# Performance work log

Measured on AMD Instinct MI355X. Metric: run time of the kernel, lower is better.

## Reference

```python
import jax, jax.numpy as jnp
from jax import lax
import numpy as np

B, NR, NC, FEAT = 8, 1024, 1024, 768
N = NR + NC
HID, GATD, GRUD = 256, 128, 64
NEG = -9e15  # matches -9000000000000000.0 in torch source


def setup_inputs() -> dict:
    key = jax.random.key(0)
    ks = jax.random.split(key, 24)
    s = 0.02
    nrm = lambda k, shp: jax.random.normal(k, shp, jnp.float32) * s
    z = lambda shp: jnp.zeros(shp, jnp.float32)
    inp = {}
    inp['req_nodes'] = jax.random.normal(ks[0], (B, NR, FEAT), jnp.float32)
    inp['code_nodes'] = jax.random.normal(ks[1], (B, NC, FEAT), jnp.float32)
    inp['alignment_matrix'] = jax.random.bernoulli(ks[2], 0.05, (B, N, N)).astype(jnp.float32)
    inp['total_nodes'] = jax.random.randint(ks[3], (B,), N // 2, N + 1).astype(jnp.int32)
    # feature_projection
    inp['W_proj'] = nrm(ks[4], (HID, FEAT)); inp['b_proj'] = z((HID,))
    # GAT layer 1 (HID->HID), attention weight a is Linear(2*HID, 1, bias=False)
    inp['W_g1'] = nrm(ks[5], (HID, HID)); inp['b_g1'] = z((HID,)); inp['a_g1'] = nrm(ks[6], (2 * HID,))
    # GAT layer 2 (HID->GATD)
    inp['W_g2'] = nrm(ks[7], (GATD, HID)); inp['b_g2'] = z((GATD,)); inp['a_g2'] = nrm(ks[8], (2 * GATD,))
    # bidirectional GRU (torch layout: [3H, in], gates r|z|n)
    inp['Wih_f'] = nrm(ks[9], (3 * GRUD, GATD)); inp['Whh_f'] = nrm(ks[10], (3 * GRUD, GRUD))
    inp['bih_f'] = z((3 * GRUD,)); inp['bhh_f'] = z((3 * GRUD,))
    inp['Wih_b'] = nrm(ks[11], (3 * GRUD, GATD)); inp['Whh_b'] = nrm(ks[12], (3 * GRUD, GRUD))
    inp['bih_b'] = z((3 * GRUD,)); inp['bhh_b'] = z((3 * GRUD,))
    inp['W_fus'] = nrm(ks[13], (GRUD, 2 * GRUD)); inp['b_fus'] = z((GRUD,))
    inp['W_c1'] = nrm(ks[14], (HID // 2, GRUD)); inp['b_c1'] = z((HID // 2,))
    inp['W_c2'] = nrm(ks[15], (1, HID // 2)); inp['b_c2'] = z((1,))
    return inp


def _gat_layer(x, adj, mask, W, b, a):
    # h: [B, N, D]
    h = x @ W.T + b
    D = h.shape[-1]
    # attention(concat(h_i, h_j)) == a[:D]@h_i + a[D:]@h_j -> never materialize [B,N,N,2D]
    s_src = h @ a[:D]   # [B, N]
    s_dst = h @ a[D:]   # [B, N]
    e = jax.nn.leaky_relu(s_src[:, :, None] + s_dst[:, None, :], 0.01)  # [B,N,N]
    att = jax.nn.softmax(jnp.where(adj > 0, e, NEG), axis=-1)
    out = jnp.einsum('bij,bjd->bid', att, h)
    return out * mask[..., None]


def _gru_dir(xproj, Whh, bhh, reverse):
    # xproj: [B, T, 3H] = x @ Wih.T + bih (precomputed)
    Bv, H = xproj.shape[0], Whh.shape[1]
    def step(h, xt):
        gh = h @ Whh.T + bhh
        ir, iz, inn = jnp.split(xt, 3, axis=-1)
        hr, hz, hn = jnp.split(gh, 3, axis=-1)
        r = jax.nn.sigmoid(ir + hr)
        zt = jax.nn.sigmoid(iz + hz)
        n = jnp.tanh(inn + r * hn)
        hnew = (1.0 - zt) * n + zt * h
        return hnew, hnew
    h0 = jnp.zeros((Bv, H), xproj.dtype)
    _, ys = lax.scan(step, h0, jnp.swapaxes(xproj, 0, 1), reverse=reverse)
    return jnp.swapaxes(ys, 0, 1)  # [B, T, H]


def _forward(req_nodes, code_nodes, alignment_matrix, total_nodes,
             W_proj, b_proj, W_g1, b_g1, a_g1, W_g2, b_g2, a_g2,
             Wih_f, Whh_f, bih_f, bhh_f, Wih_b, Whh_b, bih_b, bhh_b,
             W_fus, b_fus, W_c1, b_c1, W_c2, b_c2):
    x = jnp.concatenate([req_nodes, code_nodes], axis=1)        # [B, N, FEAT]
    proj = jax.nn.relu(x @ W_proj.T + b_proj)                   # dropout is eval-mode identity
    Nt = proj.shape[1]
    mask = (jnp.arange(Nt)[None, :] < total_nodes[:, None]).astype(proj.dtype)  # [B, N]
    g1 = _gat_layer(proj, alignment_matrix, mask, W_g1, b_g1, a_g1)
    g1 = jax.nn.relu(g1) * mask[..., None]
    gat_out = _gat_layer(g1, alignment_matrix, mask, W_g2, b_g2, a_g2)
    gat_out = gat_out * mask[..., None]  # extra masking as in torch source (idempotent)
    gf = _gru_dir(gat_out @ Wih_f.T + bih_f, Whh_f, bhh_f, reverse=False)
    gb = _gru_dir(gat_out @ Wih_b.T + bih_b, Whh_b, bhh_b, reverse=True)
    gru_out = jnp.concatenate([gf, gb], axis=-1) * mask[..., None]  # [B, N, 2*GRUD]
    fused = gru_out @ W_fus.T + b_fus                               # [B, N, GRUD]
    pooled = jnp.mean(fused, axis=1)  # AdaptiveAvgPool1d(1) over seq dim
    h1 = jax.nn.relu(pooled @ W_c1.T + b_c1)
    out = jax.nn.sigmoid(h1 @ W_c2.T + b_c2)  # [B, 1]
    return out


def reference(req_nodes, code_nodes, alignment_matrix, total_nodes,
              W_proj, b_proj, W_g1, b_g1, a_g1, W_g2, b_g2, a_g2,
              Wih_f, Whh_f, bih_f, bhh_f, Wih_b, Whh_b, bih_b, bhh_b,
              W_fus, b_fus, W_c1, b_c1, W_c2, b_c2):
    return _forward(req_nodes, code_nodes, alignment_matrix, total_nodes,
                    W_proj, b_proj, W_g1, b_g1, a_g1, W_g2, b_g2, a_g2,
                    Wih_f, Whh_f, bih_f, bhh_f, Wih_b, Whh_b, bih_b, bhh_b,
                    W_fus, b_fus, W_c1, b_c1, W_c2, b_c2)
```

## Files before the change

### kernel.cpp

```cpp
#include <hip/hip_runtime.h>
#include <stdint.h>

#define EMAX 256

typedef short bf16x8 __attribute__((ext_vector_type(8)));
typedef float f32x4 __attribute__((ext_vector_type(4)));
typedef _Float16 h2_t __attribute__((ext_vector_type(2)));

__device__ __forceinline__ uint16_t f2bf(float f) {
    union { float f; uint32_t u; } v; v.f = f;
    uint32_t u = v.u;
    uint32_t r = (u + 0x7FFFu + ((u >> 16) & 1u)) >> 16;
    return (uint16_t)r;
}
__device__ __forceinline__ float bf2f(uint16_t h) {
    union { uint32_t u; float f; } v; v.u = ((uint32_t)h) << 16;
    return v.f;
}
__device__ __forceinline__ h2_t u2h2(uint32_t u) {
    union { uint32_t u; h2_t h; } v; v.u = u;
    return v.h;
}

__global__ __launch_bounds__(256) void k_prep(const float* __restrict__ req, const float* __restrict__ code,
                                              uint16_t* __restrict__ X,
                                              const float* wp, const float* wg1, const float* wg2,
                                              const float* wif, const float* wib,
                                              const float* whf, const float* whb,
                                              const float* bihf, const float* bihb,
                                              uint16_t* op, uint16_t* og1, uint16_t* og2,
                                              uint16_t* oifb, _Float16* ohf, _Float16* ohb, float* bihfb,
                                              float* __restrict__ Sz,
                                              const float* __restrict__ adj,
                                              uint16_t* __restrict__ eidx, int* __restrict__ ecnt) {
    int blk = blockIdx.x;
    int tid = threadIdx.x;
    if (blk < 16384) {
        int b = blk >> 11, n = blk & 2047;
        if (tid < 192) {
            const float4* src4 = (const float4*)((n < 1024) ? (req  + ((size_t)(b*1024 + n)) * 768)
                                                            : (code + ((size_t)(b*1024 + (n-1024))) * 768));
            ushort4* dst4 = (ushort4*)(X + (size_t)blk * 768);
            float4 v = src4[tid];
            ushort4 p;
            p.x = f2bf(v.x); p.y = f2bf(v.y); p.z = f2bf(v.z); p.w = f2bf(v.w);
            dst4[tid] = p;
        }
    } else if (blk < 16384 + 768) {
        int i = (blk - 16384) * 256 + tid;
        if (i < 196608) op[i]  = f2bf(wp[i]);
        if (i < 65536)  og1[i] = f2bf(wg1[i]);
        if (i < 32768)  og2[i] = f2bf(wg2[i]);
        if (i < 24576)  { oifb[i] = f2bf(wif[i]); oifb[24576 + i] = f2bf(wib[i]); }
        if (i < 12288)  { ohf[i] = (_Float16)whf[i]; ohb[i] = (_Float16)whb[i]; }
        if (i < 192)    { bihfb[i] = bihf[i]; bihfb[192 + i] = bihb[i]; }
        if (i < 1024)   Sz[i] = 0.f;
    } else {
        int row  = (blk - 17152) * 4 + (tid >> 6);
        int lane = tid & 63;
        const float* arow = adj + (size_t)row * 2048;
        uint16_t* out = eidx + (size_t)row * EMAX;
        int base = 0;
        for (int c = 0; c < 32; ++c) {
            int j = c * 64 + lane;
            float v = arow[j];
            unsigned long long m = __ballot(v > 0.0f);
            if (v > 0.0f) {
                int pos = base + __popcll(m & ((1ull << lane) - 1ull));
                if (pos < EMAX) out[pos] = (uint16_t)j;
            }
            base += __popcll(m);
        }
        if (lane == 0) ecnt[row] = (base < EMAX) ? base : EMAX;
    }
}

template<int ACT, int MODE>
__global__ __launch_bounds__(256) void k_gemm(const uint16_t* __restrict__ A,
                                              const uint16_t* __restrict__ Bw,
                                              const float* __restrict__ bias,
                                              void* __restrict__ Cv, void* __restrict__ Cv2,
                                              int M, int N, int K) {
    __shared__ __align__(16) uint16_t As[64 * 64];
    __shared__ __align__(16) uint16_t Bs[64 * 64];
    int tid = threadIdx.x;
    int n0 = blockIdx.x * 64, m0 = blockIdx.y * 64;
    int wave = tid >> 6, lane = tid & 63;
    int quad = lane >> 4, l16 = lane & 15;
    f32x4 acc[4] = {};
    int ar = tid >> 3;
    int ac = (tid & 7) * 8;
    for (int kb = 0; kb < K; kb += 64) {
        *(uint4*)&As[ar * 64 + ac]        = *(const uint4*)(A  + (size_t)(m0 + ar)      * K + kb + ac);
        *(uint4*)&As[(ar + 32) * 64 + ac] = *(const uint4*)(A  + (size_t)(m0 + ar + 32) * K + kb + ac);
        *(uint4*)&Bs[ar * 64 + ac]        = *(const uint4*)(Bw + (size_t)(n0 + ar)      * K + kb + ac);
        *(uint4*)&Bs[(ar + 32) * 64 + ac] = *(const uint4*)(Bw + (size_t)(n0 + ar + 32) * K + kb + ac);
        __syncthreads();
#pragma unroll
        for (int kk = 0; kk < 64; kk += 32) {
            bf16x8 af = *(bf16x8*)&As[(wave * 16 + l16) * 64 + kk + quad * 8];
#pragma unroll
            for (int c = 0; c < 4; ++c) {
                bf16x8 bfr = *(bf16x8*)&Bs[(c * 16 + l16) * 64 + kk + quad * 8];
                acc[c] = __builtin_amdgcn_mfma_f32_16x16x32_bf16(af, bfr, acc[c], 0, 0, 0);
            }
        }
        __syncthreads();
    }
#pragma unroll
    for (int c = 0; c < 4; ++c) {
        int col = n0 + c * 16 + l16;
        float bv = bias ? bias[col] : 0.f;
#pragma unroll
        for (int rg = 0; rg < 4; ++rg) {
            int row = m0 + wave * 16 + quad * 4 + rg;
            float v = acc[c][rg] + bv;
            if (ACT == 1) v = fmaxf(v, 0.f);
            if (MODE == 1)      ((uint16_t*)Cv)[(size_t)row * N + col] = f2bf(v);
            else if (MODE == 0) ((float*)Cv)[(size_t)row * N + col] = v;
            else {
                int tc = (col < 192) ? col : col - 192;
                int dc = (tc & 63) * 4 + (tc >> 6);
                float* dst = (col < 192) ? (float*)Cv : (float*)Cv2;
                dst[(size_t)row * 256 + dc] = v;
            }
        }
    }
}

template<int D>
__global__ __launch_bounds__(256) void k_attvec(const uint16_t* __restrict__ H,
                                                const float* __restrict__ a,
                                                float* __restrict__ ssrc,
                                                float* __restrict__ sdst) {
    int row  = blockIdx.x * 4 + (threadIdx.x >> 6);
    int lane = threadIdx.x & 63;
    constexpr int PER = D >> 6;
    const uint32_t* hr = (const uint32_t*)(H + (size_t)row * D + lane * PER);
    float s0 = 0.f, s1 = 0.f;
#pragma unroll
    for (int q = 0; q < PER / 2; ++q) {
        uint32_t hv = hr[q];
        int d = lane * PER + q * 2;
        float h0 = bf2f((uint16_t)hv), h1 = bf2f((uint16_t)(hv >> 16));
        s0 += h0 * a[d] + h1 * a[d + 1];
        s1 += h0 * a[D + d] + h1 * a[D + d + 1];
    }
    for (int off = 32; off; off >>= 1) { s0 += __shfl_down(s0, off); s1 += __shfl_down(s1, off); }
    if (lane == 0) { ssrc[row] = s0; sdst[row] = s1; }
}

#define ACC4(hv, wv) { \
    a0 = fmaf(wv, bf2f((uint16_t)(hv).x), a0); \
    a1 = fmaf(wv, bf2f((uint16_t)((hv).x >> 16)), a1); \
    a2 = fmaf(wv, bf2f((uint16_t)(hv).y), a2); \
    a3 = fmaf(wv, bf2f((uint16_t)((hv).y >> 16)), a3); }

template<int D, int LAYER1>
__global__ __launch_bounds__(256) void k_agg(const uint16_t* __restrict__ H,
                                             const float* __restrict__ ssrc,
                                             const float* __restrict__ sdst,
                                             const uint16_t* __restrict__ eidx,
                                             const int* __restrict__ ecnt,
                                             const int* __restrict__ total,
                                             uint16_t* __restrict__ out) {
    constexpr int LPG = (D == 256) ? 64 : 32;
    constexpr int G   = 64 / LPG;
    constexpr int RS  = D / 4;
    __shared__ __align__(16) uint2 ew[4][EMAX];
    int tid  = threadIdx.x;
    int wid  = tid >> 6, lane = tid & 63;
    int grp  = lane / LPG;
    int c    = lane % LPG;
    int b    = blockIdx.x & 7;
    int i    = ((blockIdx.x >> 3) << 2) + wid;
    int row  = (b << 11) + i;
    uint2* orow = (uint2*)(out + (size_t)row * D);
    if (i >= total[b]) {
        if (grp == 0) { uint2 z; z.x = 0u; z.y = 0u; orow[c] = z; }
        return;
    }
    int cnt = ecnt[row];
    const uint2* H2 = (const uint2*)(H + (size_t)b * 2048 * D);
    float a0 = 0.f, a1 = 0.f, a2 = 0.f, a3 = 0.f;
    if (cnt > 0) {
        float sv = ssrc[row];
        const uint16_t* er = eidx + (size_t)row * EMAX;
        int   jj[4]; float ee[4];
#pragma unroll
        for (int k = 0; k < 4; ++k) {
            int t = lane + 64 * k;
            int j = (t < cnt) ? (int)er[t] : 0;
            float x = sv + sdst[b * 2048 + j];
            float e = (x > 0.f) ? x : 0.01f * x;
            if (t >= cnt) e = -1e30f;
            jj[k] = j; ee[k] = e;
        }
        float m = fmaxf(fmaxf(ee[0], ee[1]), fmaxf(ee[2], ee[3]));
#pragma unroll
        for (int off = 32; off; off >>= 1) m = fmaxf(m, __shfl_xor(m, off));
        float w[4]; float s = 0.f;
#pragma unroll
        for (int k = 0; k < 4; ++k) { w[k] = __expf(ee[k] - m); s += w[k]; }
#pragma unroll
        for (int off = 32; off; off >>= 1) s += __shfl_xor(s, off);
        float inv = 1.f / s;
#pragma unroll
        for (int k = 0; k < 4; ++k) {
            uint2 p; p.x = (uint32_t)jj[k]; p.y = __float_as_uint(w[k] * inv);
            ew[wid][lane + 64 * k] = p;
        }
        asm volatile("s_waitcnt lgkmcnt(0)" ::: "memory");
        constexpr int EPB = 4 * G;
        int cntP = (cnt + EPB - 1) & ~(EPB - 1);
        if constexpr (G == 1) {
            for (int t = 0; t < cntP; t += 4) {
                uint2 e0 = ew[wid][t + 0], e1 = ew[wid][t + 1];
                uint2 e2 = ew[wid][t + 2], e3 = ew[wid][t + 3];
                uint2 h0 = H2[(size_t)e0.x * RS + c];
                uint2 h1 = H2[(size_t)e1.x * RS + c];
                uint2 h2 = H2[(size_t)e2.x * RS + c];
                uint2 h3 = H2[(size_t)e3.x * RS + c];
                ACC4(h0, __uint_as_float(e0.y));
                ACC4(h1, __uint_as_float(e1.y));
                ACC4(h2, __uint_as_float(e2.y));
                ACC4(h3, __uint_as_float(e3.y));
            }
        } else {
            for (int t = 0; t < cntP; t += 8) {
                uint2 e0 = ew[wid][t + 0 + grp], e1 = ew[wid][t + 2 + grp];
                uint2 e2 = ew[wid][t + 4 + grp], e3 = ew[wid][t + 6 + grp];
                uint2 h0 = H2[(size_t)e0.x * RS + c];
                uint2 h1 = H2[(size_t)e1.x * RS + c];
                uint2 h2 = H2[(size_t)e2.x * RS + c];
                uint2 h3 = H2[(size_t)e3.x * RS + c];
                ACC4(h0, __uint_as_float(e0.y));
                ACC4(h1, __uint_as_float(e1.y));
                ACC4(h2, __uint_as_float(e2.y));
                ACC4(h3, __uint_as_float(e3.y));
            }
        }
    } else {
        for (int t = grp; t < 2048; t += G) {
            uint2 hv = H2[(size_t)t * RS + c];
            ACC4(hv, 1.f);
        }
        a0 *= (1.f / 2048.f); a1 *= (1.f / 2048.f);
        a2 *= (1.f / 2048.f); a3 *= (1.f / 2048.f);
    }
    if constexpr (G == 2) {
        a0 += __shfl_xor(a0, 32); a1 += __shfl_xor(a1, 32);
        a2 += __shfl_xor(a2, 32); a3 += __shfl_xor(a3, 32);
    }
    if (LAYER1) {
        a0 = fmaxf(a0, 0.f); a1 = fmaxf(a1, 0.f);
        a2 = fmaxf(a2, 0.f); a3 = fmaxf(a3, 0.f);
    }
    if (grp == 0) {
        uint2 pk;
        pk.x = (uint32_t)f2bf(a0) | ((uint32_t)f2bf(a1) << 16);
        pk.y = (uint32_t)f2bf(a2) | ((uint32_t)f2bf(a3) << 16);
        orow[c] = pk;
    }
}

#define CHUNKS 16
#define CLEN   128
#define WARM   64
#define FDOT2(acc, p, wq) acc = __builtin_amdgcn_fdot2(p, u2h2(wq), acc, false)
#define DOTBLK(hq, q) { \
    h2_t p0 = u2h2(hq.x), p1 = u2h2(hq.y), p2 = u2h2(hq.z), p3 = u2h2(hq.w); \
    FDOT2(ar0, p0, wr[4*q+0]); FDOT2(ar1, p1, wr[4*q+1]); FDOT2(ar2, p2, wr[4*q+2]); FDOT2(ar3, p3, wr[4*q+3]); \
    FDOT2(az0, p0, wz[4*q+0]); FDOT2(az1, p1, wz[4*q+1]); FDOT2(az2, p2, wz[4*q+2]); FDOT2(az3, p3, wz[4*q+3]); \
    FDOT2(an0, p0, wn[4*q+0]); FDOT2(an1, p1, wn[4*q+1]); FDOT2(an2, p2, wn[4*q+2]); FDOT2(an3, p3, wn[4*q+3]); }
#define GRU_STEP(xq) { \
    uint4 h0 = hv4[0], h1 = hv4[1], h2v = hv4[2], h3 = hv4[3]; \
    uint4 h4 = hv4[4], h5 = hv4[5], h6 = hv4[6], h7 = hv4[7]; \
    float ar0 = br, ar1 = 0.f, ar2 = 0.f, ar3 = 0.f; \
    float az0 = bz, az1 = 0.f, az2 = 0.f, az3 = 0.f; \
    float an0 = bn, an1 = 0.f, an2 = 0.f, an3 = 0.f; \
    DOTBLK(h0, 0) DOTBLK(h1, 1) DOTBLK(h2v, 2) DOTBLK(h3, 3) \
    DOTBLK(h4, 4) DOTBLK(h5, 5) DOTBLK(h6, 6) DOTBLK(h7, 7) \
    float ghr = (ar0 + ar1) + (ar2 + ar3); \
    float ghz = (az0 + az1) + (az2 + az3); \
    float ghn = (an0 + an1) + (an2 + an3); \
    float er = __expf(-(xq.x + ghr)); \
    float r = __builtin_amdgcn_rcpf(1.f + er); \
    float ez = __expf(-(xq.y + ghz)); \
    float z = __builtin_amdgcn_rcpf(1.f + ez); \
    float nv = fmaf(r, ghn, xq.z); \
    float en = __expf(-2.f * nv); \
    float n = fmaf(-2.f, __builtin_amdgcn_rcpf(1.f + en), 1.f); \
    hj = fmaf(z, hj - n, n); \
    sj += (t < Tcur) ? hj : 0.f; \
    hb[j] = (_Float16)hj; \
    asm volatile("" ::: "memory"); \
    t += dt; }

__global__ __attribute__((amdgpu_flat_work_group_size(64, 64), amdgpu_waves_per_eu(1, 1)))
void k_gru(const float* __restrict__ XPf, const float* __restrict__ XPb,
           const _Float16* __restrict__ WhF, const _Float16* __restrict__ WhB,
           const float* __restrict__ bhh_f, const float* __restrict__ bhh_b,
           const int* __restrict__ total,
           float* __restrict__ S) {
    int blk   = blockIdx.x;
    int chunk = blk & (CHUNKS - 1);
    int sc    = blk >> 4;
    int dir   = sc >> 3;
    int b     = sc & 7;
    int j     = threadIdx.x;
    const float* XP  = dir ? XPb : XPf;
    const uint32_t* Wd = (const uint32_t*)(dir ? WhB : WhF);
    const float* bhh = dir ? bhh_b : bhh_f;
    uint32_t wr[32], wz[32], wn[32];
#pragma unroll
    for (int c = 0; c < 32; ++c) {
        wr[c] = Wd[(size_t)(      j) * 32 + c];
        wz[c] = Wd[(size_t)( 64 + j) * 32 + c];
        wn[c] = Wd[(size_t)(128 + j) * 32 + c];
    }
    float br = bhh[j], bz = bhh[64 + j], bn = bhh[128 + j];
    __shared__ __align__(16) _Float16 hbuf[64];
    _Float16* hb = hbuf;
    hb[j] = (_Float16)0.f;
    asm volatile("s_waitcnt lgkmcnt(0)" ::: "memory");
    float hj = 0.f, sj = 0.f;
    int Tb = total[b];
    int s0 = chunk * CLEN - WARM;
    int W0 = WARM;
    if (s0 < 0) { s0 = 0; W0 = 0; }
    const float4* xbase = (const float4*)(XP + (size_t)b * 2048 * 256) + j;
    int xstep = dir ? -64 : 64;
    const float4* xptr = xbase + (size_t)(dir ? (2047 - s0) : s0) * 64;
    float4 x0 = *xptr; xptr += xstep;
    float4 x1 = *xptr; xptr += xstep;
    float4 x2 = *xptr; xptr += xstep;
    float4 x3 = *xptr; xptr += xstep;
    int t = dir ? (2047 - s0) : s0, dt = dir ? -1 : 1;
    const uint4* hv4 = (const uint4*)hb;
    int Tcur = -1;
    for (int su = 0; su < W0; su += 4) {
        GRU_STEP(x0) x0 = *xptr; xptr += xstep;
        GRU_STEP(x1) x1 = *xptr; xptr += xstep;
        GRU_STEP(x2) x2 = *xptr; xptr += xstep;
        GRU_STEP(x3) x3 = *xptr; xptr += xstep;
    }
    Tcur = Tb;
    for (int su = 0; su < CLEN; su += 4) {
        GRU_STEP(x0) x0 = *xptr; xptr += xstep;
        GRU_STEP(x1) x1 = *xptr; xptr += xstep;
        GRU_STEP(x2) x2 = *xptr; xptr += xstep;
        GRU_STEP(x3) x3 = *xptr; xptr += xstep;
    }
    atomicAdd(&S[b * 128 + dir * 64 + j], sj);
}

__global__ __launch_bounds__(128) void k_final(const float* __restrict__ S,
                                               const float* __restrict__ Wfus, const float* __restrict__ bfus,
                                               const float* __restrict__ Wc1, const float* __restrict__ bc1,
                                               const float* __restrict__ Wc2, const float* __restrict__ bc2,
                                               float* __restrict__ out) {
    __shared__ float pool[64];
    __shared__ float red[128];
    int tid = threadIdx.x;
    for (int b = 0; b < 8; ++b) {
        if (tid < 64) {
            float a = 0.f;
            for (int jj = 0; jj < 128; ++jj) a += S[b * 128 + jj] * Wfus[tid * 128 + jj];
            pool[tid] = bfus[tid] + a * (1.f / 2048.f);
        }
        __syncthreads();
        float a1 = 0.f;
        for (int d = 0; d < 64; ++d) a1 += pool[d] * Wc1[tid * 64 + d];
        float h = fmaxf(a1 + bc1[tid], 0.f);
        red[tid] = h * Wc2[tid];
        __syncthreads();
        for (int s = 64; s; s >>= 1) { if (tid < s) red[tid] += red[tid + s]; __syncthreads(); }
        if (tid == 0) out[b] = 1.f / (1.f + __expf(-(red[0] + bc2[0])));
        __syncthreads();
    }
}

extern "C" void kernel_launch(void* const* d_in, const int* in_sizes, int n_in,
                              void* d_out, int out_size, void* d_ws, size_t ws_size,
                              hipStream_t stream) {
    (void)in_sizes; (void)n_in; (void)out_size; (void)ws_size;
    const float* req   = (const float*)d_in[0];
    const float* code  = (const float*)d_in[1];
    const float* adj   = (const float*)d_in[2];
    const int*   total = (const int*)  d_in[3];
    const float* W_proj = (const float*)d_in[4];
    const float* b_proj = (const float*)d_in[5];
    const float* W_g1   = (const float*)d_in[6];
    const float* b_g1   = (const float*)d_in[7];
    const float* a_g1   = (const float*)d_in[8];
    const float* W_g2   = (const float*)d_in[9];
    const float* b_g2   = (const float*)d_in[10];
    const float* a_g2   = (const float*)d_in[11];
    const float* Wih_f  = (const float*)d_in[12];
    const float* Whh_f  = (const float*)d_in[13];
    const float* bih_f  = (const float*)d_in[14];
    const float* bhh_f  = (const float*)d_in[15];
    const float* Wih_b  = (const float*)d_in[16];
    const float* Whh_b  = (const float*)d_in[17];
    const float* bih_b  = (const float*)d_in[18];
    const float* bhh_b  = (const float*)d_in[19];
    const float* W_fus  = (const float*)d_in[20];
    const float* b_fus  = (const float*)d_in[21];
    const float* W_c1   = (const float*)d_in[22];
    const float* b_c1   = (const float*)d_in[23];
    const float* W_c2   = (const float*)d_in[24];
    const float* b_c2   = (const float*)d_in[25];

    char* ws = (char*)d_ws;
    uint16_t* Xbf  = (uint16_t*)(ws + 0);
    float*    XPf  = (float*)(ws + 4096);
    float*    XPb  = (float*)(ws + 4096 + 16777216 + 4096);
    uint16_t* EIDX = (uint16_t*)(ws + 25169920);
    uint16_t* WPb  = (uint16_t*)(ws + 33570816);
    uint16_t* WG1b = (uint16_t*)(ws + 33964032);
    uint16_t* WG2b = (uint16_t*)(ws + 34095104);
    uint16_t* WIFB = (uint16_t*)(ws + 34160640);
    uint16_t* Pbf  = (uint16_t*)(ws + 34262016);
    uint16_t* H1bf = (uint16_t*)(ws + 42650624);
    uint16_t* H2bf = (uint16_t*)(ws + 42650624);
    uint16_t* G2bf = (uint16_t*)(ws + 46844928);
    uint16_t* G1bf = (uint16_t*)(ws + 51039232);
    int*      ECNT = (int*)     (ws + 59427840);
    float* s1src = (float*)(ws + 59493376);
    float* s1dst = (float*)(ws + 59558912);
    float* s2src = (float*)(ws + 59624448);
    float* s2dst = (float*)(ws + 59689984);
    float* Sbuf  = (float*)(ws + 59755520);
    _Float16* WhFh = (_Float16*)(ws + 59759616);
    _Float16* WhBh = (_Float16*)(ws + 59784192);
    float* BIHFB   = (float*)(ws + 59808768);

    k_prep<<<21248, 256, 0, stream>>>(req, code, Xbf,
                                      W_proj, W_g1, W_g2, Wih_f, Wih_b, Whh_f, Whh_b, bih_f, bih_b,
                                      WPb, WG1b, WG2b, WIFB, WhFh, WhBh, BIHFB, Sbuf,
                                      adj, EIDX, ECNT);

    k_gemm<1, 1><<<dim3(4, 256), 256, 0, stream>>>(Xbf, WPb, b_proj, Pbf, nullptr, 16384, 256, 768);

    k_gemm<0, 1><<<dim3(4, 256), 256, 0, stream>>>(Pbf, WG1b, b_g1, H1bf, nullptr, 16384, 256, 256);
    k_attvec<256><<<4096, 256, 0, stream>>>(H1bf, a_g1, s1src, s1dst);
    k_agg<256, 1><<<4096, 256, 0, stream>>>(H1bf, s1src, s1dst, EIDX, ECNT, total, G1bf);

    k_gemm<0, 1><<<dim3(2, 256), 256, 0, stream>>>(G1bf, WG2b, b_g2, H2bf, nullptr, 16384, 128, 256);
    k_attvec<128><<<4096, 256, 0, stream>>>(H2bf, a_g2, s2src, s2dst);
    k_agg<128, 0><<<4096, 256, 0, stream>>>(H2bf, s2src, s2dst, EIDX, ECNT, total, G2bf);

    k_gemm<0, 2><<<dim3(6, 256), 256, 0, stream>>>(G2bf, WIFB, BIHFB, XPf, XPb, 16384, 384, 128);

    k_gru<<<256, 64, 0, stream>>>(XPf, XPb, WhFh, WhBh, bhh_f, bhh_b, total, Sbuf);

    k_final<<<1, 128, 0, stream>>>(Sbuf, W_fus, b_fus, W_c1, b_c1, W_c2, b_c2, (float*)d_out);
}
```

Baseline: 557.4 us.

## Fuse fp32-to-bf16 input conversion into projection GEMM and co-schedule adjacency compaction

Removes the separate pass that converted req/code features to a bf16 staging buffer. The projection GEMM now loads fp32 rows directly and packs them to bf16 with v_cvt_pk_bf16_f32 while filling shared memory. Adjacency edge-list compaction moves into the same launch as extra blocks, and each lane loads all 32 adjacency values up front. This drops a write and re-read of the staging buffer, but the GEMM's global loads double in width and weight prep becomes its own small kernel.

```diff
diff --git a/kernel.cpp b/kernel.cpp
--- a/kernel.cpp
+++ b/kernel.cpp
@@ -21,57 +21,111 @@
     union { uint32_t u; h2_t h; } v; v.u = u;
     return v.h;
 }
-
-__global__ __launch_bounds__(256) void k_prep(const float* __restrict__ req, const float* __restrict__ code,
-                                              uint16_t* __restrict__ X,
-                                              const float* wp, const float* wg1, const float* wg2,
+__device__ __forceinline__ uint32_t cvtpk_bf16(float lo, float hi) {
+    uint32_t d;
+    asm("v_cvt_pk_bf16_f32 %0, %1, %2" : "=v"(d) : "v"(lo), "v"(hi));
+    return d;
+}
+
+__global__ __launch_bounds__(256) void k_prep(const float* wp, const float* wg1, const float* wg2,
                                               const float* wif, const float* wib,
                                               const float* whf, const float* whb,
                                               const float* bihf, const float* bihb,
                                               uint16_t* op, uint16_t* og1, uint16_t* og2,
                                               uint16_t* oifb, _Float16* ohf, _Float16* ohb, float* bihfb,
-                                              float* __restrict__ Sz,
-                                              const float* __restrict__ adj,
-                                              uint16_t* __restrict__ eidx, int* __restrict__ ecnt) {
-    int blk = blockIdx.x;
+                                              float* __restrict__ Sz) {
+    int i = blockIdx.x * 256 + threadIdx.x;
+    if (i < 196608) op[i]  = f2bf(wp[i]);
+    if (i < 65536)  og1[i] = f2bf(wg1[i]);
+    if (i < 32768)  og2[i] = f2bf(wg2[i]);
+    if (i < 24576)  { oifb[i] = f2bf(wif[i]); oifb[24576 + i] = f2bf(wib[i]); }
+    if (i < 12288)  { ohf[i] = (_Float16)whf[i]; ohb[i] = (_Float16)whb[i]; }
+    if (i < 192)    { bihfb[i] = bihf[i]; bihfb[192 + i] = bihb[i]; }
+    if (i < 1024)   Sz[i] = 0.f;
+}
+
+__global__ __launch_bounds__(256) void k_g1e(const float* __restrict__ req, const float* __restrict__ code,
+                                             const uint16_t* __restrict__ Bw,
+                                             const float* __restrict__ bias,
+                                             uint16_t* __restrict__ C,
+                                             const float* __restrict__ adj,
+                                             uint16_t* __restrict__ eidx, int* __restrict__ ecnt) {
+    __shared__ __align__(16) uint16_t As[64 * 64];
+    __shared__ __align__(16) uint16_t Bs[64 * 64];
     int tid = threadIdx.x;
-    if (blk < 16384) {
-        int b = blk >> 11, n = blk & 2047;
-        if (tid < 192) {
-            const float4* src4 = (const float4*)((n < 1024) ? (req  + ((size_t)(b*1024 + n)) * 768)
-                                                            : (code + ((size_t)(b*1024 + (n-1024))) * 768));
-            ushort4* dst4 = (ushort4*)(X + (size_t)blk * 768);
-            float4 v = src4[tid];
-            ushort4 p;
-            p.x = f2bf(v.x); p.y = f2bf(v.y); p.z = f2bf(v.z); p.w = f2bf(v.w);
-            dst4[tid] = p;
-        }
-    } else if (blk < 16384 + 768) {
-        int i = (blk - 16384) * 256 + tid;
-        if (i < 196608) op[i]  = f2bf(wp[i]);
-        if (i < 65536)  og1[i] = f2bf(wg1[i]);
-        if (i < 32768)  og2[i] = f2bf(wg2[i]);
-        if (i < 24576)  { oifb[i] = f2bf(wif[i]); oifb[24576 + i] = f2bf(wib[i]); }
-        if (i < 12288)  { ohf[i] = (_Float16)whf[i]; ohb[i] = (_Float16)whb[i]; }
-        if (i < 192)    { bihfb[i] = bihf[i]; bihfb[192 + i] = bihb[i]; }
-        if (i < 1024)   Sz[i] = 0.f;
-    } else {
-        int row  = (blk - 17152) * 4 + (tid >> 6);
+    if (blockIdx.x < 4096) {
+        int row  = blockIdx.x * 4 + (tid >> 6);
         int lane = tid & 63;
-        const float* arow = adj + (size_t)row * 2048;
-        uint16_t* out = eidx + (size_t)row * EMAX;
+        const float* arow = adj + (size_t)row * 2048 + lane;
+        float v[32];
+#pragma unroll
+        for (int c = 0; c < 32; ++c) v[c] = arow[c * 64];
+        uint16_t* outr = eidx + (size_t)row * EMAX;
+        unsigned long long lt = (1ull << lane) - 1ull;
         int base = 0;
+#pragma unroll
         for (int c = 0; c < 32; ++c) {
-            int j = c * 64 + lane;
-            float v = arow[j];
-            unsigned long long m = __ballot(v > 0.0f);
-            if (v > 0.0f) {
-                int pos = base + __popcll(m & ((1ull << lane) - 1ull));
-                if (pos < EMAX) out[pos] = (uint16_t)j;
+            unsigned long long m = __ballot(v[c] > 0.f);
+            if (v[c] > 0.f) {
+                int pos = base + __popcll(m & lt);
+                if (pos < EMAX) outr[pos] = (uint16_t)(c * 64 + lane);
             }
             base += __popcll(m);
         }
         if (lane == 0) ecnt[row] = (base < EMAX) ? base : EMAX;
+        return;
+    }
+    constexpr int K = 768, N = 256;
+    int g = blockIdx.x - 4096;
+    int n0 = (g & 3) * 64, m0 = (g >> 2) * 64;
+    int wave = tid >> 6, lane = tid & 63;
+    int quad = lane >> 4, l16 = lane & 15;
+    f32x4 acc[4] = {};
+    int ar = tid >> 3;
+    int ac = (tid & 7) * 8;
+    const float4* rowp[2];
+#pragma unroll
+    for (int h = 0; h < 2; ++h) {
+        int n = m0 + ar + h * 32;
+        int b = n >> 11, n2 = n & 2047;
+        const float* s = (n2 < 1024) ? (req  + ((size_t)(b * 1024 + n2)) * 768)
+                                     : (code + ((size_t)(b * 1024 + (n2 - 1024))) * 768);
+        rowp[h] = (const float4*)s + (ac >> 2);
+    }
+    for (int kb = 0; kb < K; kb += 64) {
+#pragma unroll
+        for (int h = 0; h < 2; ++h) {
+            float4 f0 = rowp[h][(kb >> 2) + 0];
+            float4 f1 = rowp[h][(kb >> 2) + 1];
+            uint4 pk;
+            pk.x = cvtpk_bf16(f0.x, f0.y); pk.y = cvtpk_bf16(f0.z, f0.w);
+            pk.z = cvtpk_bf16(f1.x, f1.y); pk.w = cvtpk_bf16(f1.z, f1.w);
+            *(uint4*)&As[(ar + h * 32) * 64 + ac] = pk;
+        }
+        *(uint4*)&Bs[ar * 64 + ac]        = *(const uint4*)(Bw + (size_t)(n0 + ar)      * K + kb + ac);
+        *(uint4*)&Bs[(ar + 32) * 64 + ac] = *(const uint4*)(Bw + (size_t)(n0 + ar + 32) * K + kb + ac);
+        __syncthreads();
+#pragma unroll
+        for (int kk = 0; kk < 64; kk += 32) {
+            bf16x8 af = *(bf16x8*)&As[(wave * 16 + l16) * 64 + kk + quad * 8];
+#pragma unroll
+            for (int c = 0; c < 4; ++c) {
+                bf16x8 bfr = *(bf16x8*)&Bs[(c * 16 + l16) * 64 + kk + quad * 8];
+                acc[c] = __builtin_amdgcn_mfma_f32_16x16x32_bf16(af, bfr, acc[c], 0, 0, 0);
+            }
+        }
+        __syncthreads();
+    }
+#pragma unroll
+    for (int c = 0; c < 4; ++c) {
+        int col = n0 + c * 16 + l16;
+        float bv = bias[col];
+#pragma unroll
+        for (int rg = 0; rg < 4; ++rg) {
+            int row = m0 + wave * 16 + quad * 4 + rg;
+            float v = fmaxf(acc[c][rg] + bv, 0.f);
+            C[(size_t)row * N + col] = f2bf(v);
+        }
     }
 }
 
@@ -413,7 +467,6 @@
     const float* b_c2   = (const float*)d_in[25];
 
     char* ws = (char*)d_ws;
-    uint16_t* Xbf  = (uint16_t*)(ws + 0);
     float*    XPf  = (float*)(ws + 4096);
     float*    XPb  = (float*)(ws + 4096 + 16777216 + 4096);
     uint16_t* EIDX = (uint16_t*)(ws + 25169920);
@@ -436,12 +489,10 @@
     _Float16* WhBh = (_Float16*)(ws + 59784192);
     float* BIHFB   = (float*)(ws + 59808768);
 
-    k_prep<<<21248, 256, 0, stream>>>(req, code, Xbf,
-                                      W_proj, W_g1, W_g2, Wih_f, Wih_b, Whh_f, Whh_b, bih_f, bih_b,
-                                      WPb, WG1b, WG2b, WIFB, WhFh, WhBh, BIHFB, Sbuf,
-                                      adj, EIDX, ECNT);
-
-    k_gemm<1, 1><<<dim3(4, 256), 256, 0, stream>>>(Xbf, WPb, b_proj, Pbf, nullptr, 16384, 256, 768);
+    k_prep<<<768, 256, 0, stream>>>(W_proj, W_g1, W_g2, Wih_f, Wih_b, Whh_f, Whh_b, bih_f, bih_b,
+                                    WPb, WG1b, WG2b, WIFB, WhFh, WhBh, BIHFB, Sbuf);
+
+    k_g1e<<<5120, 256, 0, stream>>>(req, code, WPb, b_proj, Pbf, adj, EIDX, ECNT);
 
     k_gemm<0, 1><<<dim3(4, 256), 256, 0, stream>>>(Pbf, WG1b, b_g1, H1bf, nullptr, 16384, 256, 256);
     k_attvec<256><<<4096, 256, 0, stream>>>(H1bf, a_g1, s1src, s1dst);
```

Result: faster. 535.4 us (-3.9%).
